# Kernel tuning notes

Hardware: AMD Instinct MI355X
Metric: run time of the kernel (lower is better)

Reference implementation:

```python
import jax, jax.numpy as jnp
import numpy as np

B, S, H, F, E, K = 4, 2048, 1024, 3584, 8, 2
CAP_FACTOR = 1.25


def setup_inputs() -> dict:
    key = jax.random.key(0)
    k1, k2, k3, k4, k5 = jax.random.split(key, 5)
    s_h = 1.0 / np.sqrt(H)
    s_f = 1.0 / np.sqrt(F)
    return {
        "hidden_states": jax.random.normal(k1, (B, S, H), dtype=jnp.float32),
        "gate_w": jax.random.normal(k2, (E, H), dtype=jnp.float32) * s_h,
        "w1": jax.random.normal(k3, (E, H, F), dtype=jnp.float32) * s_h,
        "w2": jax.random.normal(k4, (E, F, H), dtype=jnp.float32) * s_f,
        "w3": jax.random.normal(k5, (E, H, F), dtype=jnp.float32) * s_h,
    }


def _moe_forward(hidden_states, gate_w, w1, w2, w3):
    b, s, h = hidden_states.shape
    dtype = hidden_states.dtype
    x = hidden_states.reshape(-1, h)  # [B*S, H]
    router_logits = x @ gate_w.T  # [B*S, E]
    expert_weights = jax.nn.softmax(router_logits.astype(jnp.float32), axis=1)
    _, selected_experts = jax.lax.top_k(expert_weights, K)  # [B*S, K]

    top_k_idx = selected_experts.reshape(b, s, K)
    probs = expert_weights.reshape(b, s, E)

    capacity = int(s * K / E * CAP_FACTOR)  # expert capacity per batch

    # dispatch/combine masks (Mixtral 'dropping' implementation)
    expert_mask = jax.nn.one_hot(top_k_idx, E, dtype=jnp.int32)  # [b,s,K,E]
    mask_fused = expert_mask.reshape(b, s * K, E)
    count_fused = jnp.cumsum(mask_fused, axis=1)  # running count per expert
    count = count_fused.reshape(b, s, K, E)
    trunc_mask = expert_mask * (count <= capacity).astype(jnp.int32)
    combined_mask = trunc_mask.sum(axis=2)  # [b,s,E]
    masked_probs = probs * combined_mask  # drop over-capacity tokens

    pos_fused = mask_fused * count_fused
    pos = pos_fused.reshape(b, s, K, E)
    combined_pos = pos.sum(axis=2) * combined_mask  # [b,s,E], 1-based slot
    pos_in_cap = jax.nn.one_hot(combined_pos, capacity + 1, dtype=jnp.int32)
    combine_mask = masked_probs[..., None] * pos_in_cap  # [b,s,E,cap+1]
    combine_mask = combine_mask[..., 1:].astype(dtype)  # drop slot 0 (dropped tokens)
    dispatch_mask = (combine_mask != 0).astype(dtype)  # [b,s,E,cap]

    # dispatch tokens into per-expert capacity buffers
    dispatch = jnp.einsum('bsm,bsec->ebcm', hidden_states, dispatch_mask)
    # expert FFN (SwiGLU)
    h1 = jnp.einsum('ebcm,emh->ebch', dispatch, w1)
    h3 = jnp.einsum('ebcm,emh->ebch', dispatch, w3)
    expert_out = jnp.einsum('ebch,ehm->ebcm', jax.nn.silu(h1) * h3, w2)
    # combine back to token order with routing probabilities
    final = jnp.einsum('ebcm,bsec->bsm', expert_out, combine_mask)
    return final


def reference(hidden_states, gate_w, w1, w2, w3):
    return _moe_forward(hidden_states, gate_w, w1, w2, w3)
```

## Files before the change

kernel.cpp:

```cpp
#include <hip/hip_runtime.h>
#include <hip/hip_bf16.h>
#include <math.h>

#define B_   4
#define S_   2048
#define H_   1024
#define F_   3584
#define E_   8
#define TOPK 2
#define CAP  640
#define M_   (B_*CAP)
#define NTOK (B_*S_)

typedef __attribute__((ext_vector_type(8))) short short8;
typedef __attribute__((ext_vector_type(4))) float f32x4;
typedef __attribute__((ext_vector_type(4))) unsigned short us4;

static __device__ __forceinline__ unsigned short f2bf(float f) {
  __hip_bfloat16 h = __float2bfloat16(f);
  return *reinterpret_cast<unsigned short*>(&h);
}
static __device__ __forceinline__ float bf2f(unsigned short u) {
  unsigned int x = ((unsigned int)u) << 16;
  float f;
  __builtin_memcpy(&f, &x, 4);
  return f;
}

static __device__ __forceinline__ void gload16(const void* g, void* l) {
  __builtin_amdgcn_global_load_lds((const __attribute__((address_space(1))) void*)g,
                                   (__attribute__((address_space(3))) void*)l, 16, 0, 0);
}

#define BAR() __builtin_amdgcn_s_barrier()
#define WLG() asm volatile("s_waitcnt lgkmcnt(0)" ::: "memory")
#define VM4() asm volatile("s_waitcnt vmcnt(4)" ::: "memory")
#define VM0() asm volatile("s_waitcnt vmcnt(0)" ::: "memory")

__global__ __launch_bounds__(64) void k_router(const float* __restrict__ hs,
                                               const float* __restrict__ gw,
                                               int* __restrict__ e01,
                                               float* __restrict__ p01) {
  int t = blockIdx.x;
  int lane = threadIdx.x;
  const float4* xv = (const float4*)(hs + (size_t)t * H_);
  float4 xr[4];
#pragma unroll
  for (int i = 0; i < 4; ++i) xr[i] = xv[lane + i * 64];
  float logit[E_];
#pragma unroll
  for (int e = 0; e < E_; ++e) {
    const float4* gv = (const float4*)(gw + (size_t)e * H_);
    float acc = 0.f;
#pragma unroll
    for (int i = 0; i < 4; ++i) {
      float4 g = gv[lane + i * 64];
      acc += xr[i].x * g.x + xr[i].y * g.y + xr[i].z * g.z + xr[i].w * g.w;
    }
#pragma unroll
    for (int off = 32; off > 0; off >>= 1) acc += __shfl_xor(acc, off);
    logit[e] = acc;
  }
  float mx = logit[0];
#pragma unroll
  for (int e = 1; e < E_; ++e) mx = fmaxf(mx, logit[e]);
  float p[E_], s = 0.f;
#pragma unroll
  for (int e = 0; e < E_; ++e) { p[e] = expf(logit[e] - mx); s += p[e]; }
  float inv = 1.f / s;
  int e0 = 0;
#pragma unroll
  for (int e = 1; e < E_; ++e) if (p[e] > p[e0]) e0 = e;
  int e1 = (e0 == 0) ? 1 : 0;
#pragma unroll
  for (int e = 0; e < E_; ++e) if (e != e0 && p[e] > p[e1]) e1 = e;
  if (lane == 0) {
    e01[t * 2 + 0] = e0;
    e01[t * 2 + 1] = e1;
    p01[t * 2 + 0] = p[e0] * inv;
    p01[t * 2 + 1] = p[e1] * inv;
  }
}

__global__ __launch_bounds__(256) void k_positions(const int* __restrict__ e01,
                                                   int* __restrict__ pos,
                                                   int* __restrict__ disp) {
  int b = blockIdx.x, tid = threadIdx.x;
  __shared__ unsigned char eid[S_ * TOPK];
  __shared__ int part[256];
  for (int i = tid; i < E_ * CAP; i += 256)
    disp[((size_t)(i / CAP) * B_ + b) * CAP + (i % CAP)] = -1;
  for (int i = tid; i < S_ * TOPK; i += 256)
    eid[i] = (unsigned char)e01[b * S_ * TOPK + i];
  __syncthreads();
  const int per = (S_ * TOPK) / 256;
  int base = tid * per;
  for (int e = 0; e < E_; ++e) {
    int cnt = 0;
    for (int j = 0; j < per; ++j) cnt += (eid[base + j] == e) ? 1 : 0;
    part[tid] = cnt;
    __syncthreads();
    for (int off = 1; off < 256; off <<= 1) {
      int v = part[tid];
      int add = (tid >= off) ? part[tid - off] : 0;
      __syncthreads();
      part[tid] = v + add;
      __syncthreads();
    }
    int run = part[tid] - cnt;
    for (int j = 0; j < per; ++j) {
      int sl = base + j;
      if (eid[sl] == e) {
        ++run;
        int p = (run <= CAP) ? (run - 1) : -1;
        pos[b * S_ * TOPK + sl] = p;
        if (p >= 0) disp[((size_t)e * B_ + b) * CAP + p] = sl >> 1;
      }
    }
    __syncthreads();
  }
}

__global__ __launch_bounds__(256) void k_cvt(const float* __restrict__ in,
                                             unsigned short* __restrict__ outp) {
  size_t i = ((size_t)blockIdx.x * 256 + threadIdx.x) * 8;
  float4 f0 = *(const float4*)&in[i];
  float4 f1 = *(const float4*)&in[i + 4];
  us4 v0 = {f2bf(f0.x), f2bf(f0.y), f2bf(f0.z), f2bf(f0.w)};
  us4 v1 = {f2bf(f1.x), f2bf(f1.y), f2bf(f1.z), f2bf(f1.w)};
  *(us4*)&outp[i] = v0;
  *(us4*)&outp[i + 4] = v1;
}

__global__ __launch_bounds__(256) void k_transpose(const float* __restrict__ in,
                                                   unsigned short* __restrict__ outp,
                                                   int R, int C, int ileave, int half,
                                                   size_t ostride_e) {
  __shared__ unsigned short ls[64][72];
  int e = blockIdx.z, tc = blockIdx.x, tr = blockIdx.y, tid = threadIdx.x;
  const float* src = in + (size_t)e * R * C + (size_t)tr * 64 * C + (size_t)tc * 64;
#pragma unroll
  for (int i = 0; i < 16; ++i) {
    int row = i * 4 + (tid >> 6), col = tid & 63;
    ls[row][col] = f2bf(src[(size_t)row * C + col]);
  }
  __syncthreads();
  unsigned short* dbase = outp + (size_t)e * ostride_e;
#pragma unroll
  for (int i = 0; i < 4; ++i) {
    int orow = i * 16 + (tid >> 4), oc = (tid & 15) * 4;
    int gr = tc * 64 + orow;
    int ri = ileave ? ((gr & ~15) * 2 + (gr & 15) + half * 16) : gr;
    us4 v = {ls[oc + 0][orow], ls[oc + 1][orow], ls[oc + 2][orow], ls[oc + 3][orow]};
    *(us4*)&dbase[(size_t)ri * R + tr * 64 + oc] = v;
  }
}

#define STAGE_A(d, h, t) {                                                    \
    size_t _o = (size_t)(t) * 64 + (h) * 32;                                  \
    gload16(pA0 + _o, &lds[((d) * 2 + (h)) * 8192 + tid * 8]);                \
    gload16(pA1 + _o, &lds[((d) * 2 + (h)) * 8192 + tid * 8 + 4096]);         \
  }
#define STAGE_B(d, h, t) {                                                    \
    size_t _o = (size_t)(t) * 64 + (h) * 32;                                  \
    gload16(srcB + _o, &lds[32768 + ((d) * 2 + (h)) * 8192 + tid * 8]);       \
    gload16(srcB + (size_t)128 * KTOT + _o, &lds[32768 + ((d) * 2 + (h)) * 8192 + tid * 8 + 4096]); \
  }
#define RD_A4(d, h, mh) {                                                     \
    const unsigned short* _pa = &lds[((d) * 2 + (h)) * 8192 + aoff + (mh) * 2048]; \
    _Pragma("unroll") for (int j = 0; j < 4; ++j)                             \
      a[j] = *(const short8*)&_pa[j * 512];                                   \
  }
#define RD_B4(d, h) {                                                         \
    const unsigned short* _pb = &lds[32768 + ((d) * 2 + (h)) * 8192 + boff];  \
    _Pragma("unroll") for (int n = 0; n < 4; ++n)                             \
      b[n] = *(const short8*)&_pb[n * 512];                                   \
  }
#define MFMA16(mh) {                                                          \
    __builtin_amdgcn_s_setprio(1);                                            \
    _Pragma("unroll") for (int j = 0; j < 4; ++j)                             \
      _Pragma("unroll") for (int n = 0; n < 4; ++n)                           \
        acc[(mh) * 4 + j][n] = __builtin_amdgcn_mfma_f32_16x16x32_bf16(a[j], b[n], acc[(mh) * 4 + j][n], 0, 0, 0); \
    __builtin_amdgcn_s_setprio(0);                                            \
  }
#define BODY(P, tn) {                                                         \
    RD_A4(P, 0, 0); RD_B4(P, 0); STAGE_A((P) ^ 1, 0, tn);                     \
    BAR(); WLG(); MFMA16(0); BAR();                                           \
    RD_A4(P, 0, 1); STAGE_B((P) ^ 1, 0, tn); VM4();                           \
    BAR(); WLG(); MFMA16(1); BAR();                                           \
    RD_A4(P, 1, 0); RD_B4(P, 1); STAGE_A((P) ^ 1, 1, tn);                     \
    BAR(); WLG(); MFMA16(0); BAR();                                           \
    RD_A4(P, 1, 1); STAGE_B((P) ^ 1, 1, tn); VM4();                           \
    BAR(); WLG(); MFMA16(1); BAR();                                           \
  }
#define PEEL(P) {                                                             \
    RD_A4(P, 0, 0); RD_B4(P, 0);                                              \
    BAR(); WLG(); MFMA16(0); BAR();                                           \
    RD_A4(P, 0, 1); VM0();                                                    \
    BAR(); WLG(); MFMA16(1); BAR();                                           \
    RD_A4(P, 1, 0); RD_B4(P, 1);                                              \
    BAR(); WLG(); MFMA16(0); BAR();                                           \
    RD_A4(P, 1, 1);                                                           \
    BAR(); WLG(); MFMA16(1);                                                  \
  }

template <int KTOT, bool SWIGLU, bool GATHER, int MT, int NTN, int NTOTB, int SPLITK>
__global__ __launch_bounds__(512, 2) void k_gemm256(const unsigned short* __restrict__ Aall,
                                                    const unsigned short* __restrict__ Ball,
                                                    unsigned short* __restrict__ Cout,
                                                    const int* __restrict__ disp) {
  constexpr int KSUB = KTOT / SPLITK;
  constexpr int NT = KSUB / 64;
  __shared__ __align__(16) unsigned short lds[65536];

  const int nwg = MT * NTN * E_ * SPLITK;
  int lid = blockIdx.x;
  int sw = (lid & 7) * (nwg >> 3) + (lid >> 3);
  constexpr int PER = MT * NTN;
  int ks = sw / (PER * E_);
  int rem2 = sw - ks * (PER * E_);
  int e = rem2 / PER;
  int rem = rem2 - e * PER;
  int tn = rem / MT, tm = rem - tn * MT;

  int tid = threadIdx.x, li = tid & 63, wid = tid >> 6;
  int wm = wid >> 1, wn = wid & 1;
  wm = wid >> 2; wn = wid & 3;

  int rS = tid >> 2;
  int gS = (tid & 3) ^ ((tid >> 3) & 3);
  const unsigned short* pA0;
  const unsigned short* pA1;
  if constexpr (GATHER) {
    int r0 = tm * 256 + rS;
    int r1 = r0 + 128;
    int b0 = r0 / CAP, b1 = r1 / CAP;
    int tok0 = disp[(size_t)e * B_ * CAP + r0];
    int tok1 = disp[(size_t)e * B_ * CAP + r1];
    if (tok0 < 0) tok0 = 0;
    if (tok1 < 0) tok1 = 0;
    pA0 = Aall + ((size_t)b0 * S_ + tok0) * H_ + ks * KSUB + gS * 8;
    pA1 = Aall + ((size_t)b1 * S_ + tok1) * H_ + ks * KSUB + gS * 8;
  } else {
    const unsigned short* srcA = Aall + ((size_t)e * M_ + (size_t)tm * 256 + rS) * KTOT + ks * KSUB + gS * 8;
    pA0 = srcA;
    pA1 = srcA + (size_t)128 * KTOT;
  }
  const unsigned short* srcB = Ball + ((size_t)e * NTOTB + (size_t)tn * 256 + rS) * KTOT + ks * KSUB + gS * 8;

  int sA = (li >> 4) ^ ((li >> 1) & 3);
  int aoff = (wm * 128 + (li & 15)) * 32 + sA * 8;
  int boff = (wn * 64 + (li & 15)) * 32 + sA * 8;

  f32x4 acc[8][4] = {};
  short8 a[4], b[4];

  STAGE_A(0, 0, 0); STAGE_B(0, 0, 0);
  STAGE_A(0, 1, 0); STAGE_B(0, 1, 0);
  VM4();
  BAR();

#pragma unroll 1
  for (int t = 0; t + 1 < NT - 1; t += 2) {
    BODY(0, t + 1);
    BODY(1, t + 2);
  }
  if constexpr (((NT - 1) & 1) != 0) {
    BODY(0, NT - 1);
  }
  if constexpr (((NT - 1) & 1) != 0) {
    PEEL(1);
  } else {
    PEEL(0);
  }

  int r0o = tm * 256 + wm * 128 + ((li >> 4) << 2);
  if constexpr (SWIGLU) {
    unsigned short* out = Cout + (size_t)e * M_ * F_;
#pragma unroll
    for (int m = 0; m < 8; ++m)
#pragma unroll
      for (int u = 0; u < 2; ++u) {
        int col = (tn * 8 + wn * 2 + u) * 16 + (li & 15);
#pragma unroll
        for (int j = 0; j < 4; ++j) {
          float h1 = acc[m][2 * u][j], h3 = acc[m][2 * u + 1][j];
          float sg = 1.f / (1.f + __expf(-h1));
          out[(size_t)(r0o + m * 16 + j) * F_ + col] = f2bf(h1 * sg * h3);
        }
      }
  } else {
    unsigned short* out = Cout + ((size_t)ks * E_ + e) * M_ * NTOTB;
#pragma unroll
    for (int m = 0; m < 8; ++m)
#pragma unroll
      for (int n = 0; n < 4; ++n) {
        int col = tn * 256 + wn * 64 + n * 16 + (li & 15);
#pragma unroll
        for (int j = 0; j < 4; ++j)
          out[(size_t)(r0o + m * 16 + j) * NTOTB + col] = f2bf(acc[m][n][j]);
      }
  }
}

__global__ __launch_bounds__(256) void k_combine(const unsigned short* __restrict__ Oe0,
                                                 const unsigned short* __restrict__ Oe1,
                                                 const int* __restrict__ e01,
                                                 const float* __restrict__ p01,
                                                 const int* __restrict__ pos,
                                                 float* __restrict__ outp) {
  int t = blockIdx.x;
  int b = t / S_;
  int tid = threadIdx.x;
  float4 acc = {0.f, 0.f, 0.f, 0.f};
#pragma unroll
  for (int k = 0; k < TOPK; ++k) {
    int p = pos[t * 2 + k];
    if (p >= 0) {
      int e = e01[t * 2 + k];
      float w = p01[t * 2 + k];
      size_t row = (size_t)e * M_ + (size_t)b * CAP + p;
      us4 v0 = *(const us4*)&Oe0[row * H_ + tid * 4];
      us4 v1 = *(const us4*)&Oe1[row * H_ + tid * 4];
      acc.x += w * (bf2f(v0[0]) + bf2f(v1[0]));
      acc.y += w * (bf2f(v0[1]) + bf2f(v1[1]));
      acc.z += w * (bf2f(v0[2]) + bf2f(v1[2]));
      acc.w += w * (bf2f(v0[3]) + bf2f(v1[3]));
    }
  }
  *(float4*)&outp[(size_t)t * H_ + tid * 4] = acc;
}

extern "C" void kernel_launch(void* const* d_in, const int* in_sizes, int n_in,
                              void* d_out, int out_size, void* d_ws, size_t ws_size,
                              hipStream_t stream) {
  const float* hs = (const float*)d_in[0];
  const float* gw = (const float*)d_in[1];
  const float* w1 = (const float*)d_in[2];
  const float* w2 = (const float*)d_in[3];
  const float* w3 = (const float*)d_in[4];

  char* ws = (char*)d_ws;
  size_t off = 0;
  auto take = [&](size_t bytes) -> char* {
    char* p = ws + off;
    off += (bytes + 255) & ~(size_t)255;
    return p;
  };
  int*            e01  = (int*)take((size_t)NTOK * 2 * 4);
  float*          p01  = (float*)take((size_t)NTOK * 2 * 4);
  int*            pos  = (int*)take((size_t)NTOK * 2 * 4);
  int*            disp = (int*)take((size_t)E_ * B_ * CAP * 4);
  unsigned short* w13t = (unsigned short*)take((size_t)E_ * 2 * F_ * H_ * 2);
  unsigned short* w2t  = (unsigned short*)take((size_t)E_ * H_ * F_ * 2);
  unsigned short* hsb  = (unsigned short*)take((size_t)NTOK * H_ * 2);
  unsigned short* act  = (unsigned short*)take((size_t)E_ * M_ * F_ * 2);
  unsigned short* oe   = (unsigned short*)take((size_t)2 * E_ * M_ * H_ * 2);

  k_router<<<NTOK, 64, 0, stream>>>(hs, gw, e01, p01);
  k_positions<<<B_, 256, 0, stream>>>(e01, pos, disp);
  k_cvt<<<(NTOK * H_) / (256 * 8), 256, 0, stream>>>(hs, hsb);
  k_transpose<<<dim3(F_ / 64, H_ / 64, E_), 256, 0, stream>>>(w1, w13t, H_, F_, 1, 0, (size_t)2 * F_ * H_);
  k_transpose<<<dim3(F_ / 64, H_ / 64, E_), 256, 0, stream>>>(w3, w13t, H_, F_, 1, 1, (size_t)2 * F_ * H_);
  k_transpose<<<dim3(H_ / 64, F_ / 64, E_), 256, 0, stream>>>(w2, w2t, F_, H_, 0, 0, (size_t)H_ * F_);
  k_gemm256<H_, true, true, M_ / 256, (2 * F_) / 256, 2 * F_, 1>
      <<<(M_ / 256) * ((2 * F_) / 256) * E_, 512, 0, stream>>>(hsb, w13t, act, disp);
  k_gemm256<F_, false, false, M_ / 256, H_ / 256, H_, 2>
      <<<(M_ / 256) * (H_ / 256) * E_ * 2, 512, 0, stream>>>(act, w2t, oe, disp);
  k_combine<<<NTOK, 256, 0, stream>>>(oe, oe + (size_t)E_ * M_ * H_, e01, p01, pos, (float*)d_out);
}
```

Measured before the change: 590.6 us.

## Fuse bf16 conversion into router and drop redundant GEMM barriers

The router kernel now writes the bf16 copy of the hidden states while it already holds them in registers, which removes the separate conversion kernel and its second read of the fp32 input. In the GEMM main loop, the barrier before each MFMA block is removed and the vmcnt wait is moved after the MFMAs, so fewer workgroup barriers sit on the critical path and global loads overlap more with compute. Removing barriers risks LDS read/write hazards if the double-buffer stage ordering does not fully protect the buffers.

```diff
diff --git a/kernel.cpp b/kernel.cpp
--- a/kernel.cpp
+++ b/kernel.cpp
@@ -40,13 +40,19 @@
 __global__ __launch_bounds__(64) void k_router(const float* __restrict__ hs,
                                                const float* __restrict__ gw,
                                                int* __restrict__ e01,
-                                               float* __restrict__ p01) {
+                                               float* __restrict__ p01,
+                                               unsigned short* __restrict__ hsb) {
   int t = blockIdx.x;
   int lane = threadIdx.x;
   const float4* xv = (const float4*)(hs + (size_t)t * H_);
   float4 xr[4];
 #pragma unroll
   for (int i = 0; i < 4; ++i) xr[i] = xv[lane + i * 64];
+#pragma unroll
+  for (int i = 0; i < 4; ++i) {
+    us4 v = {f2bf(xr[i].x), f2bf(xr[i].y), f2bf(xr[i].z), f2bf(xr[i].w)};
+    *(us4*)&hsb[(size_t)t * H_ + (size_t)(lane + i * 64) * 4] = v;
+  }
   float logit[E_];
 #pragma unroll
   for (int e = 0; e < E_; ++e) {
@@ -121,17 +127,6 @@
   }
 }
 
-__global__ __launch_bounds__(256) void k_cvt(const float* __restrict__ in,
-                                             unsigned short* __restrict__ outp) {
-  size_t i = ((size_t)blockIdx.x * 256 + threadIdx.x) * 8;
-  float4 f0 = *(const float4*)&in[i];
-  float4 f1 = *(const float4*)&in[i + 4];
-  us4 v0 = {f2bf(f0.x), f2bf(f0.y), f2bf(f0.z), f2bf(f0.w)};
-  us4 v1 = {f2bf(f1.x), f2bf(f1.y), f2bf(f1.z), f2bf(f1.w)};
-  *(us4*)&outp[i] = v0;
-  *(us4*)&outp[i + 4] = v1;
-}
-
 __global__ __launch_bounds__(256) void k_transpose(const float* __restrict__ in,
                                                    unsigned short* __restrict__ outp,
                                                    int R, int C, int ileave, int half,
@@ -185,23 +180,23 @@
   }
 #define BODY(P, tn) {                                                         \
     RD_A4(P, 0, 0); RD_B4(P, 0); STAGE_A((P) ^ 1, 0, tn);                     \
-    BAR(); WLG(); MFMA16(0); BAR();                                           \
-    RD_A4(P, 0, 1); STAGE_B((P) ^ 1, 0, tn); VM4();                           \
-    BAR(); WLG(); MFMA16(1); BAR();                                           \
+    WLG(); MFMA16(0); BAR();                                                  \
+    RD_A4(P, 0, 1); STAGE_B((P) ^ 1, 0, tn);                                  \
+    WLG(); MFMA16(1); VM4(); BAR();                                           \
     RD_A4(P, 1, 0); RD_B4(P, 1); STAGE_A((P) ^ 1, 1, tn);                     \
-    BAR(); WLG(); MFMA16(0); BAR();                                           \
-    RD_A4(P, 1, 1); STAGE_B((P) ^ 1, 1, tn); VM4();                           \
-    BAR(); WLG(); MFMA16(1); BAR();                                           \
+    WLG(); MFMA16(0); BAR();                                                  \
+    RD_A4(P, 1, 1); STAGE_B((P) ^ 1, 1, tn);                                  \
+    WLG(); MFMA16(1); VM4(); BAR();                                           \
   }
 #define PEEL(P) {                                                             \
     RD_A4(P, 0, 0); RD_B4(P, 0);                                              \
-    BAR(); WLG(); MFMA16(0); BAR();                                           \
-    RD_A4(P, 0, 1); VM0();                                                    \
-    BAR(); WLG(); MFMA16(1); BAR();                                           \
+    WLG(); MFMA16(0); BAR();                                                  \
+    RD_A4(P, 0, 1);                                                           \
+    WLG(); MFMA16(1); VM0(); BAR();                                           \
     RD_A4(P, 1, 0); RD_B4(P, 1);                                              \
-    BAR(); WLG(); MFMA16(0); BAR();                                           \
+    WLG(); MFMA16(0); BAR();                                                  \
     RD_A4(P, 1, 1);                                                           \
-    BAR(); WLG(); MFMA16(1);                                                  \
+    WLG(); MFMA16(1);                                                         \
   }
 
 template <int KTOT, bool SWIGLU, bool GATHER, int MT, int NTN, int NTOTB, int SPLITK>
@@ -224,8 +219,7 @@
   int tn = rem / MT, tm = rem - tn * MT;
 
   int tid = threadIdx.x, li = tid & 63, wid = tid >> 6;
-  int wm = wid >> 1, wn = wid & 1;
-  wm = wid >> 2; wn = wid & 3;
+  int wm = wid >> 2, wn = wid & 3;
 
   int rS = tid >> 2;
   int gS = (tid & 3) ^ ((tid >> 3) & 3);
@@ -357,9 +351,8 @@
   unsigned short* act  = (unsigned short*)take((size_t)E_ * M_ * F_ * 2);
   unsigned short* oe   = (unsigned short*)take((size_t)2 * E_ * M_ * H_ * 2);
 
-  k_router<<<NTOK, 64, 0, stream>>>(hs, gw, e01, p01);
+  k_router<<<NTOK, 64, 0, stream>>>(hs, gw, e01, p01, hsb);
   k_positions<<<B_, 256, 0, stream>>>(e01, pos, disp);
-  k_cvt<<<(NTOK * H_) / (256 * 8), 256, 0, stream>>>(hs, hsb);
   k_transpose<<<dim3(F_ / 64, H_ / 64, E_), 256, 0, stream>>>(w1, w13t, H_, F_, 1, 0, (size_t)2 * F_ * H_);
   k_transpose<<<dim3(F_ / 64, H_ / 64, E_), 256, 0, stream>>>(w3, w13t, H_, F_, 1, 1, (size_t)2 * F_ * H_);
   k_transpose<<<dim3(H_ / 64, F_ / 64, E_), 256, 0, stream>>>(w2, w2t, F_, H_, 0, 0, (size_t)H_ * F_);
```

After: 576.4 us. -2.4%, faster.
